# Optimization experiments

Measured on AMD Instinct MI355X. Metric: run time of the kernel, lower is better.

The kernel has to match this reference:

```python
import jax, jax.numpy as jnp
import numpy as np

DIM_IN = 64
DIM_OUT = 64
SCALE = DIM_IN ** (-0.5)

def setup_inputs() -> dict:
    key = jax.random.key(0)
    ks = jax.random.split(key, 9)
    B, C, N, S = 4, DIM_IN, 16384, 16
    inp = {
        "xyz": jax.random.normal(ks[0], (B, 3, N), jnp.float32),
        "neighbor_xyz": jax.random.normal(ks[1], (B, 3, N, S), jnp.float32),
        "point": jax.random.normal(ks[2], (B, C, N), jnp.float32),
        "neighbor_points": jax.random.normal(ks[3], (B, C, N, S), jnp.float32),
        "neighbor_cost": jax.random.normal(ks[4], (B, C, N, S), jnp.float32),
        # 1x1 conv weights (kernel dims squeezed): [out_ch, in_ch]
        "w_k": jax.random.normal(ks[5], (DIM_IN, DIM_IN), jnp.float32) * (DIM_IN ** -0.5),
        "w_v": jax.random.normal(ks[6], (DIM_OUT, DIM_IN), jnp.float32) * (DIM_IN ** -0.5),
        "w_pos": jax.random.normal(ks[7], (DIM_IN, 4), jnp.float32) * 0.5,
        "b_pos": jax.random.normal(ks[8], (DIM_IN,), jnp.float32) * 0.01,
    }
    return inp

def reference(xyz, neighbor_xyz, point, neighbor_points, neighbor_cost, w_k, w_v, w_pos, b_pos):
    # xyz: [B,3,N]; neighbor_xyz: [B,3,N,S]; point: [B,C,N]; neighbor_cost: [B,C,N,S]
    tmp = xyz[:, :, :, None] - neighbor_xyz                      # [B,3,N,S]
    xyz_norm = jnp.linalg.norm(tmp, axis=1, keepdims=True)       # [B,1,N,S]
    pos = jnp.concatenate([tmp, xyz_norm], axis=1)               # [B,4,N,S]
    pos_enc = jnp.einsum('oc,bcns->bons', w_pos, pos) + b_pos[None, :, None, None]
    k = jnp.einsum('oc,bcns->bons', w_k, neighbor_cost + pos_enc)  # [B,C,N,S]
    v = jnp.einsum('oc,bcns->bons', w_v, neighbor_cost)            # [B,Co,N,S]
    q = point * SCALE                                              # note: self.q conv unused in original
    attn = jnp.einsum('bcn,bcns->bns', q, k)                       # channel-reduced scores
    attn = jax.nn.softmax(attn, axis=-1)                           # softmax over S neighbors
    out = jnp.einsum('bns,bcns->bcn', attn, v)                     # [B,Co,N]
    return out
```

## Files before the change

kernel.cpp:

```cpp
#include <hip/hip_runtime.h>

#define NCH    64
#define NPTS   16384
#define NS     16
#define QSCALE 0.125f

__global__ __launch_bounds__(256, 4) void pt_attn_kernel(
    const float* __restrict__ xyz,
    const float* __restrict__ nxyz,
    const float* __restrict__ point,
    const float* __restrict__ cost,
    const float* __restrict__ w_k,
    const float* __restrict__ w_v,
    const float* __restrict__ w_pos,
    const float* __restrict__ b_pos,
    float* __restrict__ out)
{
    __shared__ float wmat[64][68];
    __shared__ float ptq[64][16];
    __shared__ float qp[16][68];
    __shared__ float wpb[5][65];
    __shared__ float qg[5][16];
    __shared__ float linit[4][64];
    __shared__ float wc[16][68];

    const int t  = threadIdx.x;
    const int b  = blockIdx.x >> 10;
    const int n0 = (blockIdx.x & 1023) << 4;

    const float* point_b = point + (size_t)b * NCH * NPTS;
    const float* cost_b  = cost  + (size_t)b * NCH * NPTS * NS;
    const float* xyz_b   = xyz   + (size_t)b * 3 * NPTS;
    const float* nxyz_b  = nxyz  + (size_t)b * 3 * NPTS * NS;
    float*       out_b   = out   + (size_t)b * NCH * NPTS;

    const int w    = __builtin_amdgcn_readfirstlane(t >> 6);
    const int lane = t & 63;

#pragma unroll
    for (int i = 0; i < 16; ++i) {
        int idx = t + i * 256;
        wmat[idx >> 6][idx & 63] = w_k[idx];
    }
#pragma unroll
    for (int i = 0; i < 4; ++i) {
        int idx = t + i * 256;
        ptq[idx >> 4][idx & 15] = point_b[(idx >> 4) * NPTS + n0 + (idx & 15)] * QSCALE;
    }
    wpb[t & 3][t >> 2] = w_pos[t];
    if (t < 64) wpb[4][t] = b_pos[t];
    __syncthreads();

    {
        const int nl = t & 15, cg = t >> 4;
        float a0 = 0.f, a1 = 0.f, a2 = 0.f, a3 = 0.f;
#pragma unroll 8
        for (int o = 0; o < NCH; ++o) {
            float pvv = ptq[o][nl];
            float4 wk = *(const float4*)&wmat[o][cg * 4];
            a0 = fmaf(wk.x, pvv, a0);
            a1 = fmaf(wk.y, pvv, a1);
            a2 = fmaf(wk.z, pvv, a2);
            a3 = fmaf(wk.w, pvv, a3);
        }
        float4 r; r.x = a0; r.y = a1; r.z = a2; r.w = a3;
        *(float4*)&qp[nl][cg * 4] = r;
    }
    __syncthreads();

    if (t < 80) {
        const int j = t >> 4, nl = t & 15;
        float a = 0.f;
#pragma unroll 8
        for (int c = 0; c < NCH; ++c)
            a = fmaf(qp[nl][c], wpb[j][c], a);
        qg[j][nl] = a;
    }
#pragma unroll
    for (int i = 0; i < 16; ++i) {
        int idx = t + i * 256;
        wmat[idx & 63][idx >> 6] = w_v[idx];
    }
    __syncthreads();

    const int n0w = n0 + (w << 2);
    const int c2  = lane >> 4;
    const int nn  = (lane >> 2) & 3;
    const int s4  = lane & 3;
    const int gn  = lane >> 4;
    const int gs  = lane & 15;

    float gx0 = xyz_b[0 * NPTS + n0w + gn];
    float gx1 = xyz_b[1 * NPTS + n0w + gn];
    float gx2 = xyz_b[2 * NPTS + n0w + gn];
    float ga0 = nxyz_b[(size_t)(0 * NPTS + n0w + gn) * NS + gs];
    float ga1 = nxyz_b[(size_t)(1 * NPTS + n0w + gn) * NS + gs];
    float ga2 = nxyz_b[(size_t)(2 * NPTS + n0w + gn) * NS + gs];

    const float4* cbase = (const float4*)(cost_b + (size_t)(n0w + nn) * NS) + s4;
    float4 cr[16];
#pragma unroll
    for (int g = 0; g < 16; ++g)
        cr[g] = cbase[(size_t)(g * 4 + c2) * NPTS * 4];

    {
        float t0 = gx0 - ga0, t1 = gx1 - ga1, t2 = gx2 - ga2;
        float nr = sqrtf(fmaf(t0, t0, fmaf(t1, t1, t2 * t2)));
        int nlg = (w << 2) + gn;
        float li = fmaf(qg[0][nlg], t0, fmaf(qg[1][nlg], t1,
                   fmaf(qg[2][nlg], t2, fmaf(qg[3][nlg], nr, qg[4][nlg]))));
        linit[w][lane] = li;
    }
    float4 lg = *(const float4*)&linit[w][nn * 16 + s4 * 4];
    if (c2 != 0) { lg.x = 0.f; lg.y = 0.f; lg.z = 0.f; lg.w = 0.f; }

    const int nl = (w << 2) + nn;
#pragma unroll
    for (int g = 0; g < 16; ++g) {
        float qv = qp[nl][g * 4 + c2];
        lg.x = fmaf(qv, cr[g].x, lg.x);
        lg.y = fmaf(qv, cr[g].y, lg.y);
        lg.z = fmaf(qv, cr[g].z, lg.z);
        lg.w = fmaf(qv, cr[g].w, lg.w);
    }
    lg.x += __shfl_xor(lg.x, 16); lg.y += __shfl_xor(lg.y, 16);
    lg.z += __shfl_xor(lg.z, 16); lg.w += __shfl_xor(lg.w, 16);
    lg.x += __shfl_xor(lg.x, 32); lg.y += __shfl_xor(lg.y, 32);
    lg.z += __shfl_xor(lg.z, 32); lg.w += __shfl_xor(lg.w, 32);

    float m = fmaxf(fmaxf(lg.x, lg.y), fmaxf(lg.z, lg.w));
    m = fmaxf(m, __shfl_xor(m, 1));
    m = fmaxf(m, __shfl_xor(m, 2));
    float4 at;
    at.x = __expf(lg.x - m); at.y = __expf(lg.y - m);
    at.z = __expf(lg.z - m); at.w = __expf(lg.w - m);
    float Z = at.x + at.y + at.z + at.w;
    Z += __shfl_xor(Z, 1);
    Z += __shfl_xor(Z, 2);
    float rz = 1.f / Z;
    at.x *= rz; at.y *= rz; at.z *= rz; at.w *= rz;

    float pv[16];
#pragma unroll
    for (int g = 0; g < 16; ++g) {
        float p = fmaf(at.x, cr[g].x, fmaf(at.y, cr[g].y,
                  fmaf(at.z, cr[g].z, at.w * cr[g].w)));
        p += __shfl_xor(p, 1);
        p += __shfl_xor(p, 2);
        pv[g] = p;
    }
    if (s4 == 0) {
#pragma unroll
        for (int g = 0; g < 16; ++g)
            wc[nl][g * 4 + c2] = pv[g];
    }
    __syncthreads();

    {
        const int og = t >> 4, nlo = t & 15;
        float a0 = 0.f, a1 = 0.f, a2 = 0.f, a3 = 0.f;
#pragma unroll 8
        for (int c = 0; c < NCH; ++c) {
            float wcv = wc[nlo][c];
            float4 wv = *(const float4*)&wmat[c][og * 4];
            a0 = fmaf(wv.x, wcv, a0);
            a1 = fmaf(wv.y, wcv, a1);
            a2 = fmaf(wv.z, wcv, a2);
            a3 = fmaf(wv.w, wcv, a3);
        }
        float* op = out_b + (size_t)(og * 4) * NPTS + n0 + nlo;
        op[0]        = a0;
        op[NPTS]     = a1;
        op[2 * NPTS] = a2;
        op[3 * NPTS] = a3;
    }
}

extern "C" void kernel_launch(void* const* d_in, const int* in_sizes, int n_in,
                              void* d_out, int out_size, void* d_ws, size_t ws_size,
                              hipStream_t stream) {
    const float* xyz   = (const float*)d_in[0];
    const float* nxyz  = (const float*)d_in[1];
    const float* point = (const float*)d_in[2];
    const float* cost  = (const float*)d_in[4];
    const float* w_k   = (const float*)d_in[5];
    const float* w_v   = (const float*)d_in[6];
    const float* w_pos = (const float*)d_in[7];
    const float* b_pos = (const float*)d_in[8];
    float* outp = (float*)d_out;

    dim3 grid(4096), block(256);
    hipLaunchKernelGGL(pt_attn_kernel, grid, block, 0, stream,
                       xyz, nxyz, point, cost, w_k, w_v, w_pos, b_pos, outp);
}
```

Before: 498.2 us.

## Hoist all global loads to kernel start and defer w_v staging past softmax

```diff
diff --git a/kernel.cpp b/kernel.cpp
--- a/kernel.cpp
+++ b/kernel.cpp
@@ -4,6 +4,8 @@
 #define NPTS   16384
 #define NS     16
 #define QSCALE 0.125f
+
+#define BARRIER() asm volatile("s_waitcnt lgkmcnt(0)\n\ts_barrier" ::: "memory")
 
 __global__ __launch_bounds__(256, 4) void pt_attn_kernel(
     const float* __restrict__ xyz,
@@ -18,7 +20,7 @@
 {
     __shared__ float wmat[64][68];
     __shared__ float ptq[64][16];
-    __shared__ float qp[16][68];
+    __shared__ float qp2[16][76];
     __shared__ float wpb[5][65];
     __shared__ float qg[5][16];
     __shared__ float linit[4][64];
@@ -37,19 +39,48 @@
     const int w    = __builtin_amdgcn_readfirstlane(t >> 6);
     const int lane = t & 63;
 
+    float wkv[16];
+#pragma unroll
+    for (int i = 0; i < 16; ++i) wkv[i] = w_k[t + i * 256];
+    float ptv[4];
+#pragma unroll
+    for (int i = 0; i < 4; ++i) {
+        int idx = t + i * 256;
+        ptv[i] = point_b[(idx >> 4) * NPTS + n0 + (idx & 15)];
+    }
+    float wpv = w_pos[t & 255];
+    float bpv = (t < 64) ? b_pos[t] : 0.f;
+    const int n0w = n0 + (w << 2);
+    const int gn  = lane >> 4;
+    const int gs  = lane & 15;
+    float gx0 = xyz_b[0 * NPTS + n0w + gn];
+    float gx1 = xyz_b[1 * NPTS + n0w + gn];
+    float gx2 = xyz_b[2 * NPTS + n0w + gn];
+    float ga0 = nxyz_b[(size_t)(0 * NPTS + n0w + gn) * NS + gs];
+    float ga1 = nxyz_b[(size_t)(1 * NPTS + n0w + gn) * NS + gs];
+    float ga2 = nxyz_b[(size_t)(2 * NPTS + n0w + gn) * NS + gs];
+    const int c2 = lane >> 4;
+    const int nn = (lane >> 2) & 3;
+    const int s4 = lane & 3;
+    const float4* cbase = (const float4*)(cost_b + (size_t)(n0w + nn) * NS) + s4;
+    float4 cr[16];
+#pragma unroll
+    for (int g = 0; g < 16; ++g)
+        cr[g] = cbase[(size_t)(g * 4 + c2) * NPTS * 4];
+
 #pragma unroll
     for (int i = 0; i < 16; ++i) {
         int idx = t + i * 256;
-        wmat[idx >> 6][idx & 63] = w_k[idx];
+        wmat[idx >> 6][idx & 63] = wkv[i];
     }
 #pragma unroll
     for (int i = 0; i < 4; ++i) {
         int idx = t + i * 256;
-        ptq[idx >> 4][idx & 15] = point_b[(idx >> 4) * NPTS + n0 + (idx & 15)] * QSCALE;
-    }
-    wpb[t & 3][t >> 2] = w_pos[t];
-    if (t < 64) wpb[4][t] = b_pos[t];
-    __syncthreads();
+        ptq[idx >> 4][idx & 15] = ptv[i] * QSCALE;
+    }
+    wpb[t & 3][t >> 2] = wpv;
+    if (t < 64) wpb[4][t] = bpv;
+    BARRIER();
 
     {
         const int nl = t & 15, cg = t >> 4;
@@ -63,45 +94,22 @@
             a2 = fmaf(wk.z, pvv, a2);
             a3 = fmaf(wk.w, pvv, a3);
         }
-        float4 r; r.x = a0; r.y = a1; r.z = a2; r.w = a3;
-        *(float4*)&qp[nl][cg * 4] = r;
-    }
-    __syncthreads();
+        qp2[nl][0 * 16 + cg] = a0;
+        qp2[nl][1 * 16 + cg] = a1;
+        qp2[nl][2 * 16 + cg] = a2;
+        qp2[nl][3 * 16 + cg] = a3;
+    }
+    BARRIER();
 
     if (t < 80) {
         const int j = t >> 4, nl = t & 15;
         float a = 0.f;
 #pragma unroll 8
         for (int c = 0; c < NCH; ++c)
-            a = fmaf(qp[nl][c], wpb[j][c], a);
+            a = fmaf(qp2[nl][(c & 3) * 16 + (c >> 2)], wpb[j][c], a);
         qg[j][nl] = a;
     }
-#pragma unroll
-    for (int i = 0; i < 16; ++i) {
-        int idx = t + i * 256;
-        wmat[idx & 63][idx >> 6] = w_v[idx];
-    }
-    __syncthreads();
-
-    const int n0w = n0 + (w << 2);
-    const int c2  = lane >> 4;
-    const int nn  = (lane >> 2) & 3;
-    const int s4  = lane & 3;
-    const int gn  = lane >> 4;
-    const int gs  = lane & 15;
-
-    float gx0 = xyz_b[0 * NPTS + n0w + gn];
-    float gx1 = xyz_b[1 * NPTS + n0w + gn];
-    float gx2 = xyz_b[2 * NPTS + n0w + gn];
-    float ga0 = nxyz_b[(size_t)(0 * NPTS + n0w + gn) * NS + gs];
-    float ga1 = nxyz_b[(size_t)(1 * NPTS + n0w + gn) * NS + gs];
-    float ga2 = nxyz_b[(size_t)(2 * NPTS + n0w + gn) * NS + gs];
-
-    const float4* cbase = (const float4*)(cost_b + (size_t)(n0w + nn) * NS) + s4;
-    float4 cr[16];
-#pragma unroll
-    for (int g = 0; g < 16; ++g)
-        cr[g] = cbase[(size_t)(g * 4 + c2) * NPTS * 4];
+    BARRIER();
 
     {
         float t0 = gx0 - ga0, t1 = gx1 - ga1, t2 = gx2 - ga2;
@@ -115,13 +123,26 @@
     if (c2 != 0) { lg.x = 0.f; lg.y = 0.f; lg.z = 0.f; lg.w = 0.f; }
 
     const int nl = (w << 2) + nn;
-#pragma unroll
-    for (int g = 0; g < 16; ++g) {
-        float qv = qp[nl][g * 4 + c2];
-        lg.x = fmaf(qv, cr[g].x, lg.x);
-        lg.y = fmaf(qv, cr[g].y, lg.y);
-        lg.z = fmaf(qv, cr[g].z, lg.z);
-        lg.w = fmaf(qv, cr[g].w, lg.w);
+    const float* qrow = &qp2[nl][c2 * 16];
+#pragma unroll
+    for (int k = 0; k < 4; ++k) {
+        float4 qv = *(const float4*)(qrow + 4 * k);
+        lg.x = fmaf(qv.x, cr[4 * k + 0].x, lg.x);
+        lg.y = fmaf(qv.x, cr[4 * k + 0].y, lg.y);
+        lg.z = fmaf(qv.x, cr[4 * k + 0].z, lg.z);
+        lg.w = fmaf(qv.x, cr[4 * k + 0].w, lg.w);
+        lg.x = fmaf(qv.y, cr[4 * k + 1].x, lg.x);
+        lg.y = fmaf(qv.y, cr[4 * k + 1].y, lg.y);
+        lg.z = fmaf(qv.y, cr[4 * k + 1].z, lg.z);
+        lg.w = fmaf(qv.y, cr[4 * k + 1].w, lg.w);
+        lg.x = fmaf(qv.z, cr[4 * k + 2].x, lg.x);
+        lg.y = fmaf(qv.z, cr[4 * k + 2].y, lg.y);
+        lg.z = fmaf(qv.z, cr[4 * k + 2].z, lg.z);
+        lg.w = fmaf(qv.z, cr[4 * k + 2].w, lg.w);
+        lg.x = fmaf(qv.w, cr[4 * k + 3].x, lg.x);
+        lg.y = fmaf(qv.w, cr[4 * k + 3].y, lg.y);
+        lg.z = fmaf(qv.w, cr[4 * k + 3].z, lg.z);
+        lg.w = fmaf(qv.w, cr[4 * k + 3].w, lg.w);
     }
     lg.x += __shfl_xor(lg.x, 16); lg.y += __shfl_xor(lg.y, 16);
     lg.z += __shfl_xor(lg.z, 16); lg.w += __shfl_xor(lg.w, 16);
@@ -140,21 +161,21 @@
     float rz = 1.f / Z;
     at.x *= rz; at.y *= rz; at.z *= rz; at.w *= rz;
 
-    float pv[16];
 #pragma unroll
     for (int g = 0; g < 16; ++g) {
         float p = fmaf(at.x, cr[g].x, fmaf(at.y, cr[g].y,
                   fmaf(at.z, cr[g].z, at.w * cr[g].w)));
         p += __shfl_xor(p, 1);
         p += __shfl_xor(p, 2);
-        pv[g] = p;
-    }
-    if (s4 == 0) {
-#pragma unroll
-        for (int g = 0; g < 16; ++g)
-            wc[nl][g * 4 + c2] = pv[g];
-    }
-    __syncthreads();
+        if (s4 == 0) wc[nl][g * 4 + c2] = p;
+    }
+
+#pragma unroll
+    for (int i = 0; i < 16; ++i) {
+        int idx = t + i * 256;
+        wmat[idx & 63][idx >> 6] = w_v[idx];
+    }
+    BARRIER();
 
     {
         const int og = t >> 4, nlo = t & 15;
```

Result: no change. 500.9 us (+0.5%).
